# Performance work log

Measured on AMD Instinct MI355X. Metric: run time of the kernel, lower is better.

The kernel has to match this reference:

```python
import jax, jax.numpy as jnp
import numpy as np

WINDOW_SIZE = 11
SIGMA = 1.5
C1 = 0.01 ** 2
C2 = 0.03 ** 2
ALPHA = 0.84


def _gaussian_window(window_size, sigma):
    x = np.arange(window_size, dtype=np.float32)
    g = np.exp(-((x - window_size // 2) ** 2) / (2.0 * sigma ** 2))
    g = g / g.sum()
    w2d = np.outer(g, g).astype(np.float32)  # [K, K]
    return jnp.asarray(w2d)


def _depthwise_conv(x, window):
    # x: [B, C, H, W]; window: [K, K] shared across channels (depthwise)
    C = x.shape[1]
    K = window.shape[0]
    kern = jnp.broadcast_to(window[None, None], (C, 1, K, K))  # [C, 1, K, K] OIHW
    pad = K // 2
    return jax.lax.conv_general_dilated(
        x, kern,
        window_strides=(1, 1),
        padding=((pad, pad), (pad, pad)),
        dimension_numbers=('NCHW', 'OIHW', 'NCHW'),
        feature_group_count=C,
    )


def _ssim(img1, img2):
    window = _gaussian_window(WINDOW_SIZE, SIGMA)
    mu1 = _depthwise_conv(img1, window)
    mu2 = _depthwise_conv(img2, window)
    mu1_sq = mu1 * mu1
    mu2_sq = mu2 * mu2
    mu1_mu2 = mu1 * mu2
    sigma1_sq = _depthwise_conv(img1 * img1, window) - mu1_sq
    sigma2_sq = _depthwise_conv(img2 * img2, window) - mu2_sq
    sigma12 = _depthwise_conv(img1 * img2, window) - mu1_mu2
    ssim_map = ((2 * mu1_mu2 + C1) * (2 * sigma12 + C2)) / (
        (mu1_sq + mu2_sq + C1) * (sigma1_sq + sigma2_sq + C2))
    return ssim_map.mean()


def setup_inputs() -> dict:
    key = jax.random.key(0)
    k1, k2 = jax.random.split(key)
    shape = (32, 3, 512, 512)
    pred = jax.random.uniform(k1, shape, dtype=jnp.float32)
    target = jax.random.uniform(k2, shape, dtype=jnp.float32)
    return {"pred": pred, "target": target}


def reference(pred, target):
    l1 = jnp.mean(jnp.abs(pred - target))
    s = _ssim(pred, target)
    return ALPHA * l1 + (1.0 - ALPHA) * (1.0 - s)
```

## Files before the change

kernel.cpp:

```cpp
#include <hip/hip_runtime.h>

#define SSIM_H 512
#define SSIM_W 512
#define PLANES 96
#define TILE 64
#define GRID_X (SSIM_W / TILE)
#define GRID_Y (SSIM_H / TILE)
#define TOTAL_BLOCKS (GRID_X * GRID_Y * PLANES)
#define N_TOTAL 25165824.0

typedef _Float16 half4v __attribute__((ext_vector_type(4)));
typedef _Float16 half8v __attribute__((ext_vector_type(8)));
typedef float float4v __attribute__((ext_vector_type(4)));

struct __align__(16) d2 { double x, y; };

__device__ __forceinline__ float gwf(int k) {
  const float d = (float)(k - 5);
  return __expf(-d * d / 4.5f) * 0.26601171702936207f;
}

__global__ __launch_bounds__(256, 3)
void ssim_l1_kernel(const float* __restrict__ pred,
                    const float* __restrict__ targ,
                    double* __restrict__ partials) {
  __shared__ _Float16 Hs[5][64][84];
  __shared__ float red[2][4];

  const int tid = (int)threadIdx.x;
  const int wv = tid >> 6;
  const int lane = tid & 63;
  const int q = lane >> 4;
  const int m = lane & 15;

  const int tr0 = (int)blockIdx.y * TILE;
  const int tc0 = (int)blockIdx.x * TILE;
  const size_t pbase = (size_t)blockIdx.z * (SSIM_H * SSIM_W);
  const float* __restrict__ xp = pred + pbase;
  const float* __restrict__ yp = targ + pbase;

  half8v wf;
#pragma unroll
  for (int j = 0; j < 8; ++j) {
    const int k = 8 * q + j - m;
    const float v = (k >= 0 && k <= 10) ? gwf(k) : 0.0f;
    wf[j] = (_Float16)v;
  }

  float l1 = 0.0f;

  {
    const int cw = tc0 + 16 * wv;
    const int cbase = cw - 5 + 8 * q;
    const bool cfast = (cbase >= 0) && (cbase + 7 < SSIM_W);

#pragma unroll
    for (int rg = 0; rg < 5; ++rg) {
      const int grow = tr0 - 5 + rg * 16 + m;
      float xf[8], yf[8];
      if ((unsigned)grow < (unsigned)SSIM_H) {
        const float* __restrict__ xr = xp + (size_t)grow * SSIM_W;
        const float* __restrict__ yr = yp + (size_t)grow * SSIM_W;
        if (cfast) {
          float4 a0, a1, b0, b1;
          __builtin_memcpy(&a0, xr + cbase, 16);
          __builtin_memcpy(&a1, xr + cbase + 4, 16);
          __builtin_memcpy(&b0, yr + cbase, 16);
          __builtin_memcpy(&b1, yr + cbase + 4, 16);
          xf[0] = a0.x; xf[1] = a0.y; xf[2] = a0.z; xf[3] = a0.w;
          xf[4] = a1.x; xf[5] = a1.y; xf[6] = a1.z; xf[7] = a1.w;
          yf[0] = b0.x; yf[1] = b0.y; yf[2] = b0.z; yf[3] = b0.w;
          yf[4] = b1.x; yf[5] = b1.y; yf[6] = b1.z; yf[7] = b1.w;
        } else {
#pragma unroll
          for (int j = 0; j < 8; ++j) {
            const int c = cbase + j;
            const bool ok = (unsigned)c < (unsigned)SSIM_W;
            xf[j] = ok ? xr[c] : 0.0f;
            yf[j] = ok ? yr[c] : 0.0f;
          }
        }
      } else {
#pragma unroll
        for (int j = 0; j < 8; ++j) { xf[j] = 0.0f; yf[j] = 0.0f; }
      }

      const int hr = rg * 16 + m;
      if (hr >= 5 && hr < 69) {
#pragma unroll
        for (int j = 0; j < 8; ++j) {
          const int k = 8 * q + j;
          if (k >= 5 && k < 21) l1 += fabsf(xf[j] - yf[j]);
        }
      }

      half8v ax, ay, axx, ayy, axy;
#pragma unroll
      for (int j = 0; j < 8; ++j) {
        ax[j]  = (_Float16)xf[j];
        ay[j]  = (_Float16)yf[j];
        axx[j] = (_Float16)(xf[j] * xf[j]);
        ayy[j] = (_Float16)(yf[j] * yf[j]);
        axy[j] = (_Float16)(xf[j] * yf[j]);
      }
      const float4v z = {0.0f, 0.0f, 0.0f, 0.0f};
      float4v c0 = __builtin_amdgcn_mfma_f32_16x16x32_f16(ax,  wf, z, 0, 0, 0);
      float4v c1 = __builtin_amdgcn_mfma_f32_16x16x32_f16(ay,  wf, z, 0, 0, 0);
      float4v c2 = __builtin_amdgcn_mfma_f32_16x16x32_f16(axx, wf, z, 0, 0, 0);
      float4v c3 = __builtin_amdgcn_mfma_f32_16x16x32_f16(ayy, wf, z, 0, 0, 0);
      float4v c4 = __builtin_amdgcn_mfma_f32_16x16x32_f16(axy, wf, z, 0, 0, 0);

      const int hcol = 16 * wv + m;
      const int hrow = rg * 16 + 4 * q;
      half4v h;
      h[0] = (_Float16)c0[0]; h[1] = (_Float16)c0[1];
      h[2] = (_Float16)c0[2]; h[3] = (_Float16)c0[3];
      *(half4v*)&Hs[0][hcol][hrow] = h;
      h[0] = (_Float16)c1[0]; h[1] = (_Float16)c1[1];
      h[2] = (_Float16)c1[2]; h[3] = (_Float16)c1[3];
      *(half4v*)&Hs[1][hcol][hrow] = h;
      h[0] = (_Float16)c2[0]; h[1] = (_Float16)c2[1];
      h[2] = (_Float16)c2[2]; h[3] = (_Float16)c2[3];
      *(half4v*)&Hs[2][hcol][hrow] = h;
      h[0] = (_Float16)c3[0]; h[1] = (_Float16)c3[1];
      h[2] = (_Float16)c3[2]; h[3] = (_Float16)c3[3];
      *(half4v*)&Hs[3][hcol][hrow] = h;
      h[0] = (_Float16)c4[0]; h[1] = (_Float16)c4[1];
      h[2] = (_Float16)c4[2]; h[3] = (_Float16)c4[3];
      *(half4v*)&Hs[4][hcol][hrow] = h;
    }
  }

  __syncthreads();

  float ssim = 0.0f;
  {
    const float C1v = 1.0e-4f, C2v = 9.0e-4f;
#pragma unroll
    for (int cg = 0; cg < 4; ++cg) {
      const int hcol = 16 * cg + m;
      const int hrow = 16 * wv + 8 * q;
      const float4v z = {0.0f, 0.0f, 0.0f, 0.0f};
      float4v acc[5];
#pragma unroll
      for (int p = 0; p < 5; ++p) {
        const _Float16* hp = &Hs[p][hcol][hrow];
        half4v lo = *(const half4v*)hp;
        half4v hi = *(const half4v*)(hp + 4);
        half8v bf = __builtin_shufflevector(lo, hi, 0, 1, 2, 3, 4, 5, 6, 7);
        acc[p] = __builtin_amdgcn_mfma_f32_16x16x32_f16(wf, bf, z, 0, 0, 0);
      }
#pragma unroll
      for (int r = 0; r < 4; ++r) {
        const float mu1 = acc[0][r], mu2 = acc[1][r];
        const float exx = acc[2][r], eyy = acc[3][r], exy = acc[4][r];
        const float m11 = mu1 * mu1, m22 = mu2 * mu2, m12 = mu1 * mu2;
        const float num = (2.0f * m12 + C1v) * (2.0f * (exy - m12) + C2v);
        const float den = (m11 + m22 + C1v) *
                          ((exx - m11) + (eyy - m22) + C2v);
        ssim += num / den;
      }
    }
  }

  float v0 = l1, v1 = ssim;
#pragma unroll
  for (int off = 32; off > 0; off >>= 1) {
    v0 += __shfl_down(v0, off, 64);
    v1 += __shfl_down(v1, off, 64);
  }
  if (lane == 0) { red[0][wv] = v0; red[1][wv] = v1; }
  __syncthreads();
  if (tid == 0) {
    d2 s;
    s.x = (double)red[0][0] + (double)red[0][1] +
          (double)red[0][2] + (double)red[0][3];
    s.y = (double)red[1][0] + (double)red[1][1] +
          (double)red[1][2] + (double)red[1][3];
    const int bid = ((int)blockIdx.z * GRID_Y + (int)blockIdx.y) * GRID_X +
                    (int)blockIdx.x;
    *(d2*)(partials + 2 * bid) = s;
  }
}

__global__ __launch_bounds__(256)
void finalize_kernel(const double* __restrict__ partials,
                     float* __restrict__ out) {
  __shared__ double red[2][4];
  const int tid = (int)threadIdx.x;
  double L = 0.0, S = 0.0;
  for (int i = tid; i < TOTAL_BLOCKS; i += 256) {
    const d2 v = *(const d2*)(partials + 2 * i);
    L += v.x;
    S += v.y;
  }
#pragma unroll
  for (int off = 32; off > 0; off >>= 1) {
    L += __shfl_down(L, off, 64);
    S += __shfl_down(S, off, 64);
  }
  const int lane = tid & 63, wid = tid >> 6;
  if (lane == 0) { red[0][wid] = L; red[1][wid] = S; }
  __syncthreads();
  if (tid == 0) {
    const double Ls = red[0][0] + red[0][1] + red[0][2] + red[0][3];
    const double Ss = red[1][0] + red[1][1] + red[1][2] + red[1][3];
    const double invN = 1.0 / N_TOTAL;
    out[0] = (float)(0.84 * (Ls * invN) + 0.16 * (1.0 - Ss * invN));
  }
}

extern "C" void kernel_launch(void* const* d_in, const int* in_sizes, int n_in,
                              void* d_out, int out_size, void* d_ws, size_t ws_size,
                              hipStream_t stream) {
  const float* pred = (const float*)d_in[0];
  const float* targ = (const float*)d_in[1];
  float* out = (float*)d_out;
  double* partials = (double*)d_ws;

  dim3 grid(GRID_X, GRID_Y, PLANES);
  ssim_l1_kernel<<<grid, 256, 0, stream>>>(pred, targ, partials);
  finalize_kernel<<<1, 256, 0, stream>>>(partials, out);
}
```

Measured before the change: 276.1 us.

## Hoist all global loads, make vertical pass wave-local, drop block barrier

All five row-group global loads now issue up front, with a fast unguarded path for interior tiles, so memory latency overlaps before the horizontal MFMA work. The vertical pass is remapped so each wave reads only the Hs columns it wrote itself. That lets the __syncthreads be replaced by a local LDS waitcnt, and the LDS reads are batched ahead of the MFMAs. The cost is higher register pressure from holding 80 floats per thread, which may reduce occupancy under launch_bounds(256,3).

```diff
diff --git a/kernel.cpp b/kernel.cpp
--- a/kernel.cpp
+++ b/kernel.cpp
@@ -47,17 +47,33 @@
     wf[j] = (_Float16)v;
   }
 
-  float l1 = 0.0f;
-
-  {
-    const int cw = tc0 + 16 * wv;
-    const int cbase = cw - 5 + 8 * q;
-    const bool cfast = (cbase >= 0) && (cbase + 7 < SSIM_W);
-
+  const int cw = tc0 + 16 * wv;
+  const int cbase = cw - 5 + 8 * q;
+
+  float xf[5][8], yf[5][8];
+  const bool interior = (tr0 >= 5) && (tr0 + 74 < SSIM_H) &&
+                        (tc0 >= 5) && (tc0 + 74 < SSIM_W);
+  if (interior) {
 #pragma unroll
     for (int rg = 0; rg < 5; ++rg) {
       const int grow = tr0 - 5 + rg * 16 + m;
-      float xf[8], yf[8];
+      const float* __restrict__ xr = xp + (size_t)grow * SSIM_W;
+      const float* __restrict__ yr = yp + (size_t)grow * SSIM_W;
+      float4 a0, a1, b0, b1;
+      __builtin_memcpy(&a0, xr + cbase, 16);
+      __builtin_memcpy(&a1, xr + cbase + 4, 16);
+      __builtin_memcpy(&b0, yr + cbase, 16);
+      __builtin_memcpy(&b1, yr + cbase + 4, 16);
+      xf[rg][0] = a0.x; xf[rg][1] = a0.y; xf[rg][2] = a0.z; xf[rg][3] = a0.w;
+      xf[rg][4] = a1.x; xf[rg][5] = a1.y; xf[rg][6] = a1.z; xf[rg][7] = a1.w;
+      yf[rg][0] = b0.x; yf[rg][1] = b0.y; yf[rg][2] = b0.z; yf[rg][3] = b0.w;
+      yf[rg][4] = b1.x; yf[rg][5] = b1.y; yf[rg][6] = b1.z; yf[rg][7] = b1.w;
+    }
+  } else {
+    const bool cfast = (cbase >= 0) && (cbase + 7 < SSIM_W);
+#pragma unroll
+    for (int rg = 0; rg < 5; ++rg) {
+      const int grow = tr0 - 5 + rg * 16 + m;
       if ((unsigned)grow < (unsigned)SSIM_H) {
         const float* __restrict__ xr = xp + (size_t)grow * SSIM_W;
         const float* __restrict__ yr = yp + (size_t)grow * SSIM_W;
@@ -67,89 +83,101 @@
           __builtin_memcpy(&a1, xr + cbase + 4, 16);
           __builtin_memcpy(&b0, yr + cbase, 16);
           __builtin_memcpy(&b1, yr + cbase + 4, 16);
-          xf[0] = a0.x; xf[1] = a0.y; xf[2] = a0.z; xf[3] = a0.w;
-          xf[4] = a1.x; xf[5] = a1.y; xf[6] = a1.z; xf[7] = a1.w;
-          yf[0] = b0.x; yf[1] = b0.y; yf[2] = b0.z; yf[3] = b0.w;
-          yf[4] = b1.x; yf[5] = b1.y; yf[6] = b1.z; yf[7] = b1.w;
+          xf[rg][0] = a0.x; xf[rg][1] = a0.y; xf[rg][2] = a0.z; xf[rg][3] = a0.w;
+          xf[rg][4] = a1.x; xf[rg][5] = a1.y; xf[rg][6] = a1.z; xf[rg][7] = a1.w;
+          yf[rg][0] = b0.x; yf[rg][1] = b0.y; yf[rg][2] = b0.z; yf[rg][3] = b0.w;
+          yf[rg][4] = b1.x; yf[rg][5] = b1.y; yf[rg][6] = b1.z; yf[rg][7] = b1.w;
         } else {
 #pragma unroll
           for (int j = 0; j < 8; ++j) {
             const int c = cbase + j;
             const bool ok = (unsigned)c < (unsigned)SSIM_W;
-            xf[j] = ok ? xr[c] : 0.0f;
-            yf[j] = ok ? yr[c] : 0.0f;
+            xf[rg][j] = ok ? xr[c] : 0.0f;
+            yf[rg][j] = ok ? yr[c] : 0.0f;
           }
         }
       } else {
 #pragma unroll
-        for (int j = 0; j < 8; ++j) { xf[j] = 0.0f; yf[j] = 0.0f; }
-      }
-
-      const int hr = rg * 16 + m;
-      if (hr >= 5 && hr < 69) {
-#pragma unroll
-        for (int j = 0; j < 8; ++j) {
-          const int k = 8 * q + j;
-          if (k >= 5 && k < 21) l1 += fabsf(xf[j] - yf[j]);
-        }
-      }
-
-      half8v ax, ay, axx, ayy, axy;
+        for (int j = 0; j < 8; ++j) { xf[rg][j] = 0.0f; yf[rg][j] = 0.0f; }
+      }
+    }
+  }
+
+  float l1 = 0.0f;
+#pragma unroll
+  for (int rg = 0; rg < 5; ++rg) {
+    const int hr = rg * 16 + m;
+    if (hr >= 5 && hr < 69) {
 #pragma unroll
       for (int j = 0; j < 8; ++j) {
-        ax[j]  = (_Float16)xf[j];
-        ay[j]  = (_Float16)yf[j];
-        axx[j] = (_Float16)(xf[j] * xf[j]);
-        ayy[j] = (_Float16)(yf[j] * yf[j]);
-        axy[j] = (_Float16)(xf[j] * yf[j]);
-      }
-      const float4v z = {0.0f, 0.0f, 0.0f, 0.0f};
-      float4v c0 = __builtin_amdgcn_mfma_f32_16x16x32_f16(ax,  wf, z, 0, 0, 0);
-      float4v c1 = __builtin_amdgcn_mfma_f32_16x16x32_f16(ay,  wf, z, 0, 0, 0);
-      float4v c2 = __builtin_amdgcn_mfma_f32_16x16x32_f16(axx, wf, z, 0, 0, 0);
-      float4v c3 = __builtin_amdgcn_mfma_f32_16x16x32_f16(ayy, wf, z, 0, 0, 0);
-      float4v c4 = __builtin_amdgcn_mfma_f32_16x16x32_f16(axy, wf, z, 0, 0, 0);
-
-      const int hcol = 16 * wv + m;
-      const int hrow = rg * 16 + 4 * q;
-      half4v h;
-      h[0] = (_Float16)c0[0]; h[1] = (_Float16)c0[1];
-      h[2] = (_Float16)c0[2]; h[3] = (_Float16)c0[3];
-      *(half4v*)&Hs[0][hcol][hrow] = h;
-      h[0] = (_Float16)c1[0]; h[1] = (_Float16)c1[1];
-      h[2] = (_Float16)c1[2]; h[3] = (_Float16)c1[3];
-      *(half4v*)&Hs[1][hcol][hrow] = h;
-      h[0] = (_Float16)c2[0]; h[1] = (_Float16)c2[1];
-      h[2] = (_Float16)c2[2]; h[3] = (_Float16)c2[3];
-      *(half4v*)&Hs[2][hcol][hrow] = h;
-      h[0] = (_Float16)c3[0]; h[1] = (_Float16)c3[1];
-      h[2] = (_Float16)c3[2]; h[3] = (_Float16)c3[3];
-      *(half4v*)&Hs[3][hcol][hrow] = h;
-      h[0] = (_Float16)c4[0]; h[1] = (_Float16)c4[1];
-      h[2] = (_Float16)c4[2]; h[3] = (_Float16)c4[3];
-      *(half4v*)&Hs[4][hcol][hrow] = h;
-    }
-  }
-
-  __syncthreads();
+        const int k = 8 * q + j;
+        if (k >= 5 && k < 21) l1 += fabsf(xf[rg][j] - yf[rg][j]);
+      }
+    }
+
+    half8v ax, ay, axx, ayy, axy;
+#pragma unroll
+    for (int j = 0; j < 8; ++j) {
+      const float x = xf[rg][j], y = yf[rg][j];
+      ax[j]  = (_Float16)x;
+      ay[j]  = (_Float16)y;
+      axx[j] = (_Float16)(x * x);
+      ayy[j] = (_Float16)(y * y);
+      axy[j] = (_Float16)(x * y);
+    }
+    const float4v z = {0.0f, 0.0f, 0.0f, 0.0f};
+    float4v c0 = __builtin_amdgcn_mfma_f32_16x16x32_f16(ax,  wf, z, 0, 0, 0);
+    float4v c1 = __builtin_amdgcn_mfma_f32_16x16x32_f16(ay,  wf, z, 0, 0, 0);
+    float4v c2 = __builtin_amdgcn_mfma_f32_16x16x32_f16(axx, wf, z, 0, 0, 0);
+    float4v c3 = __builtin_amdgcn_mfma_f32_16x16x32_f16(ayy, wf, z, 0, 0, 0);
+    float4v c4 = __builtin_amdgcn_mfma_f32_16x16x32_f16(axy, wf, z, 0, 0, 0);
+
+    const int hcol = 16 * wv + m;
+    const int hrow = rg * 16 + 4 * q;
+    half4v h;
+    h[0] = (_Float16)c0[0]; h[1] = (_Float16)c0[1];
+    h[2] = (_Float16)c0[2]; h[3] = (_Float16)c0[3];
+    *(half4v*)&Hs[0][hcol][hrow] = h;
+    h[0] = (_Float16)c1[0]; h[1] = (_Float16)c1[1];
+    h[2] = (_Float16)c1[2]; h[3] = (_Float16)c1[3];
+    *(half4v*)&Hs[1][hcol][hrow] = h;
+    h[0] = (_Float16)c2[0]; h[1] = (_Float16)c2[1];
+    h[2] = (_Float16)c2[2]; h[3] = (_Float16)c2[3];
+    *(half4v*)&Hs[2][hcol][hrow] = h;
+    h[0] = (_Float16)c3[0]; h[1] = (_Float16)c3[1];
+    h[2] = (_Float16)c3[2]; h[3] = (_Float16)c3[3];
+    *(half4v*)&Hs[3][hcol][hrow] = h;
+    h[0] = (_Float16)c4[0]; h[1] = (_Float16)c4[1];
+    h[2] = (_Float16)c4[2]; h[3] = (_Float16)c4[3];
+    *(half4v*)&Hs[4][hcol][hrow] = h;
+  }
+
+  asm volatile("s_waitcnt lgkmcnt(0)" ::: "memory");
 
   float ssim = 0.0f;
   {
-    const float C1v = 1.0e-4f, C2v = 9.0e-4f;
-#pragma unroll
-    for (int cg = 0; cg < 4; ++cg) {
-      const int hcol = 16 * cg + m;
-      const int hrow = 16 * wv + 8 * q;
-      const float4v z = {0.0f, 0.0f, 0.0f, 0.0f};
-      float4v acc[5];
+    const int hcol = 16 * wv + m;
+    half8v bfr[4][5];
+#pragma unroll
+    for (int rb = 0; rb < 4; ++rb) {
+      const int hrow = 16 * rb + 8 * q;
 #pragma unroll
       for (int p = 0; p < 5; ++p) {
         const _Float16* hp = &Hs[p][hcol][hrow];
         half4v lo = *(const half4v*)hp;
         half4v hi = *(const half4v*)(hp + 4);
-        half8v bf = __builtin_shufflevector(lo, hi, 0, 1, 2, 3, 4, 5, 6, 7);
-        acc[p] = __builtin_amdgcn_mfma_f32_16x16x32_f16(wf, bf, z, 0, 0, 0);
-      }
+        bfr[rb][p] = __builtin_shufflevector(lo, hi, 0, 1, 2, 3, 4, 5, 6, 7);
+      }
+    }
+    const float C1v = 1.0e-4f, C2v = 9.0e-4f;
+#pragma unroll
+    for (int rb = 0; rb < 4; ++rb) {
+      const float4v z = {0.0f, 0.0f, 0.0f, 0.0f};
+      float4v acc[5];
+#pragma unroll
+      for (int p = 0; p < 5; ++p)
+        acc[p] = __builtin_amdgcn_mfma_f32_16x16x32_f16(wf, bfr[rb][p], z,
+                                                        0, 0, 0);
 #pragma unroll
       for (int r = 0; r < 4; ++r) {
         const float mu1 = acc[0][r], mu2 = acc[1][r];
```

Result: no change. 270.8 us (-1.9%).

## Merge x²+y² blur channel, keep vertical pass wave-local, and shrink LDS

Applied to the files above, without the earlier changes.

The E[x²] and E[y²] blurs are combined into one convolution of x²+y², because SSIM only uses their sum. This cuts the MFMA count per pass from 5 to 4 and the LDS planes from 5 to 4. Each wave now does the vertical pass on the same columns it wrote, so __syncthreads is replaced with an LDS waitcnt and a sched barrier. Combined with trimming the LDS row padding, this lets occupancy rise from 3 to 4 blocks per CU. The risks are extra fp16 rounding error on the summed squares and reliance on wave-local LDS visibility.

```diff
diff --git a/kernel.cpp b/kernel.cpp
--- a/kernel.cpp
+++ b/kernel.cpp
@@ -20,11 +20,11 @@
   return __expf(-d * d / 4.5f) * 0.26601171702936207f;
 }
 
-__global__ __launch_bounds__(256, 3)
+__global__ __launch_bounds__(256, 4)
 void ssim_l1_kernel(const float* __restrict__ pred,
                     const float* __restrict__ targ,
                     double* __restrict__ partials) {
-  __shared__ _Float16 Hs[5][64][84];
+  __shared__ _Float16 Hs[4][64][76];
   __shared__ float red[2][4];
 
   const int tid = (int)threadIdx.x;
@@ -47,69 +47,68 @@
     wf[j] = (_Float16)v;
   }
 
+  const int cw = tc0 + 16 * wv;
+  const int cbase = cw - 5 + 8 * q;
+  const bool cfast = (cbase >= 0) && (cbase + 7 < SSIM_W);
+
   float l1 = 0.0f;
 
-  {
-    const int cw = tc0 + 16 * wv;
-    const int cbase = cw - 5 + 8 * q;
-    const bool cfast = (cbase >= 0) && (cbase + 7 < SSIM_W);
-
-#pragma unroll
-    for (int rg = 0; rg < 5; ++rg) {
-      const int grow = tr0 - 5 + rg * 16 + m;
-      float xf[8], yf[8];
-      if ((unsigned)grow < (unsigned)SSIM_H) {
-        const float* __restrict__ xr = xp + (size_t)grow * SSIM_W;
-        const float* __restrict__ yr = yp + (size_t)grow * SSIM_W;
-        if (cfast) {
-          float4 a0, a1, b0, b1;
-          __builtin_memcpy(&a0, xr + cbase, 16);
-          __builtin_memcpy(&a1, xr + cbase + 4, 16);
-          __builtin_memcpy(&b0, yr + cbase, 16);
-          __builtin_memcpy(&b1, yr + cbase + 4, 16);
-          xf[0] = a0.x; xf[1] = a0.y; xf[2] = a0.z; xf[3] = a0.w;
-          xf[4] = a1.x; xf[5] = a1.y; xf[6] = a1.z; xf[7] = a1.w;
-          yf[0] = b0.x; yf[1] = b0.y; yf[2] = b0.z; yf[3] = b0.w;
-          yf[4] = b1.x; yf[5] = b1.y; yf[6] = b1.z; yf[7] = b1.w;
-        } else {
-#pragma unroll
-          for (int j = 0; j < 8; ++j) {
-            const int c = cbase + j;
-            const bool ok = (unsigned)c < (unsigned)SSIM_W;
-            xf[j] = ok ? xr[c] : 0.0f;
-            yf[j] = ok ? yr[c] : 0.0f;
-          }
+#pragma unroll
+  for (int rg = 0; rg < 5; ++rg) {
+    const int grow = tr0 - 5 + rg * 16 + m;
+    float xf[8], yf[8];
+    if ((unsigned)grow < (unsigned)SSIM_H) {
+      const float* __restrict__ xr = xp + (size_t)grow * SSIM_W;
+      const float* __restrict__ yr = yp + (size_t)grow * SSIM_W;
+      if (cfast) {
+        float4 a0, a1, b0, b1;
+        __builtin_memcpy(&a0, xr + cbase, 16);
+        __builtin_memcpy(&a1, xr + cbase + 4, 16);
+        __builtin_memcpy(&b0, yr + cbase, 16);
+        __builtin_memcpy(&b1, yr + cbase + 4, 16);
+        xf[0] = a0.x; xf[1] = a0.y; xf[2] = a0.z; xf[3] = a0.w;
+        xf[4] = a1.x; xf[5] = a1.y; xf[6] = a1.z; xf[7] = a1.w;
+        yf[0] = b0.x; yf[1] = b0.y; yf[2] = b0.z; yf[3] = b0.w;
+        yf[4] = b1.x; yf[5] = b1.y; yf[6] = b1.z; yf[7] = b1.w;
+      } else {
+#pragma unroll
+        for (int j = 0; j < 8; ++j) {
+          const int c = cbase + j;
+          const bool ok = (unsigned)c < (unsigned)SSIM_W;
+          xf[j] = ok ? xr[c] : 0.0f;
+          yf[j] = ok ? yr[c] : 0.0f;
         }
-      } else {
-#pragma unroll
-        for (int j = 0; j < 8; ++j) { xf[j] = 0.0f; yf[j] = 0.0f; }
-      }
-
-      const int hr = rg * 16 + m;
-      if (hr >= 5 && hr < 69) {
-#pragma unroll
-        for (int j = 0; j < 8; ++j) {
-          const int k = 8 * q + j;
-          if (k >= 5 && k < 21) l1 += fabsf(xf[j] - yf[j]);
-        }
-      }
-
-      half8v ax, ay, axx, ayy, axy;
+      }
+    } else {
+#pragma unroll
+      for (int j = 0; j < 8; ++j) { xf[j] = 0.0f; yf[j] = 0.0f; }
+    }
+
+    const int hr = rg * 16 + m;
+    if (hr >= 5 && hr < 69) {
 #pragma unroll
       for (int j = 0; j < 8; ++j) {
-        ax[j]  = (_Float16)xf[j];
-        ay[j]  = (_Float16)yf[j];
-        axx[j] = (_Float16)(xf[j] * xf[j]);
-        ayy[j] = (_Float16)(yf[j] * yf[j]);
-        axy[j] = (_Float16)(xf[j] * yf[j]);
-      }
-      const float4v z = {0.0f, 0.0f, 0.0f, 0.0f};
-      float4v c0 = __builtin_amdgcn_mfma_f32_16x16x32_f16(ax,  wf, z, 0, 0, 0);
-      float4v c1 = __builtin_amdgcn_mfma_f32_16x16x32_f16(ay,  wf, z, 0, 0, 0);
-      float4v c2 = __builtin_amdgcn_mfma_f32_16x16x32_f16(axx, wf, z, 0, 0, 0);
-      float4v c3 = __builtin_amdgcn_mfma_f32_16x16x32_f16(ayy, wf, z, 0, 0, 0);
-      float4v c4 = __builtin_amdgcn_mfma_f32_16x16x32_f16(axy, wf, z, 0, 0, 0);
-
+        const int k = 8 * q + j;
+        if (k >= 5 && k < 21) l1 += fabsf(xf[j] - yf[j]);
+      }
+    }
+
+    half8v ax, ay, axxyy, axy;
+#pragma unroll
+    for (int j = 0; j < 8; ++j) {
+      const float x = xf[j], y = yf[j];
+      ax[j]    = (_Float16)x;
+      ay[j]    = (_Float16)y;
+      axxyy[j] = (_Float16)(x * x + y * y);
+      axy[j]   = (_Float16)(x * y);
+    }
+    const float4v z = {0.0f, 0.0f, 0.0f, 0.0f};
+    float4v c0 = __builtin_amdgcn_mfma_f32_16x16x32_f16(ax,    wf, z, 0, 0, 0);
+    float4v c1 = __builtin_amdgcn_mfma_f32_16x16x32_f16(ay,    wf, z, 0, 0, 0);
+    float4v c2 = __builtin_amdgcn_mfma_f32_16x16x32_f16(axxyy, wf, z, 0, 0, 0);
+    float4v c3 = __builtin_amdgcn_mfma_f32_16x16x32_f16(axy,   wf, z, 0, 0, 0);
+
+    if (rg != 4 || q != 3) {
       const int hcol = 16 * wv + m;
       const int hrow = rg * 16 + 4 * q;
       half4v h;
@@ -125,39 +124,44 @@
       h[0] = (_Float16)c3[0]; h[1] = (_Float16)c3[1];
       h[2] = (_Float16)c3[2]; h[3] = (_Float16)c3[3];
       *(half4v*)&Hs[3][hcol][hrow] = h;
-      h[0] = (_Float16)c4[0]; h[1] = (_Float16)c4[1];
-      h[2] = (_Float16)c4[2]; h[3] = (_Float16)c4[3];
-      *(half4v*)&Hs[4][hcol][hrow] = h;
-    }
-  }
-
-  __syncthreads();
+    }
+  }
+
+  asm volatile("s_waitcnt lgkmcnt(0)" ::: "memory");
+  __builtin_amdgcn_sched_barrier(0);
 
   float ssim = 0.0f;
   {
+    const int hcol = 16 * wv + m;
+    half8v bfr[4][4];
+#pragma unroll
+    for (int rb = 0; rb < 4; ++rb) {
+      const int hrow = 16 * rb + 8 * q;
+      const int hrow_hi = (hrow + 4 <= 72) ? hrow + 4 : 72;
+#pragma unroll
+      for (int p = 0; p < 4; ++p) {
+        half4v lo = *(const half4v*)&Hs[p][hcol][hrow];
+        half4v hi = *(const half4v*)&Hs[p][hcol][hrow_hi];
+        bfr[rb][p] = __builtin_shufflevector(lo, hi, 0, 1, 2, 3, 4, 5, 6, 7);
+      }
+    }
     const float C1v = 1.0e-4f, C2v = 9.0e-4f;
 #pragma unroll
-    for (int cg = 0; cg < 4; ++cg) {
-      const int hcol = 16 * cg + m;
-      const int hrow = 16 * wv + 8 * q;
+    for (int rb = 0; rb < 4; ++rb) {
       const float4v z = {0.0f, 0.0f, 0.0f, 0.0f};
-      float4v acc[5];
-#pragma unroll
-      for (int p = 0; p < 5; ++p) {
-        const _Float16* hp = &Hs[p][hcol][hrow];
-        half4v lo = *(const half4v*)hp;
-        half4v hi = *(const half4v*)(hp + 4);
-        half8v bf = __builtin_shufflevector(lo, hi, 0, 1, 2, 3, 4, 5, 6, 7);
-        acc[p] = __builtin_amdgcn_mfma_f32_16x16x32_f16(wf, bf, z, 0, 0, 0);
-      }
+      float4v acc[4];
+#pragma unroll
+      for (int p = 0; p < 4; ++p)
+        acc[p] = __builtin_amdgcn_mfma_f32_16x16x32_f16(wf, bfr[rb][p], z,
+                                                        0, 0, 0);
 #pragma unroll
       for (int r = 0; r < 4; ++r) {
         const float mu1 = acc[0][r], mu2 = acc[1][r];
-        const float exx = acc[2][r], eyy = acc[3][r], exy = acc[4][r];
+        const float exxyy = acc[2][r], exy = acc[3][r];
         const float m11 = mu1 * mu1, m22 = mu2 * mu2, m12 = mu1 * mu2;
         const float num = (2.0f * m12 + C1v) * (2.0f * (exy - m12) + C2v);
         const float den = (m11 + m22 + C1v) *
-                          ((exx - m11) + (eyy - m22) + C2v);
+                          ((exxyy - m11 - m22) + C2v);
         ssim += num / den;
       }
     }
```

Result: faster. 252.2 us (-8.6%).
